# Kernel tuning notes

Measured on AMD Instinct MI355X. Metric: run time of the kernel, lower is better.

## Reference

```python
import jax, jax.numpy as jnp
import numpy as np

TEMP = 0.07
BASE_TEMP = 0.07


def setup_inputs() -> dict:
    key = jax.random.key(0)
    k1, k2 = jax.random.split(key)
    B, L, D = 512, 20, 128  # batch, num_classes, feat_size
    features = jax.random.normal(k1, (B, L, D), dtype=jnp.float32)
    # contrastive features are typically L2-normalized projections
    features = features / jnp.linalg.norm(features, axis=-1, keepdims=True)
    labels = jax.random.randint(k2, (B, L), 0, 2).astype(jnp.int32)  # multi-hot
    return {"features": features, "labels": labels}


def reference(features, labels):
    # features: [B, L, D], labels: [B, L] multi-hot
    B, L, D = features.shape
    dt = features.dtype
    lab = labels.astype(dt).T                      # [L, B]
    feat = jnp.transpose(features, (1, 0, 2))      # [L, B, D]

    logits_mask = 1.0 - jnp.eye(B, dtype=dt)       # [B, B], zero diagonal
    # mask[c, i, j] = labels[i, c] * labels[j, c] * (i != j)
    mask = (lab[:, :, None] * lab[:, None, :]) * logits_mask  # [L, B, B]

    # anchor_dot_contrast[c, l, i, j] = f[l,i] . f[c,j] / T  -> exp, masked on (i,j)
    # Compute via one big N x N gram, N = L*B (same math, single GEMM).
    F = feat.reshape(L * B, D)
    E = jnp.exp((F @ F.T) / jnp.asarray(TEMP, dt)).reshape(L, B, L, B)  # E[l,i,c,j]
    tot = E.sum(axis=(0, 3))                       # [B(i), L(c)] : sum over l, all j
    diag = jnp.diagonal(E, axis1=1, axis2=3)       # [L(l), L(c), B(i)] : j == i terms
    # sum_exp_logits[c, i] = sum_{l, j != i} exp(f[l,i].f[c,j]/T)
    S = tot.T - diag.sum(axis=0)                   # [L(c), B(i)]

    # numerator[c, i, j] = f[c,i] . f[c,j] / T
    numerator = jnp.einsum('cid,cjd->cij', feat, feat) / jnp.asarray(TEMP, dt)  # [L,B,B]
    log_prob = numerator - jnp.log(S)[:, :, None]  # [L, B, B]

    mean_log_prob_pos = (mask * log_prob).sum(axis=(0, 2))  # [B]
    average = mask.sum(axis=(0, 2))                          # [B]
    average = jnp.where(average == 0, jnp.asarray(1.0, dt), average)
    mean_log_prob_pos = mean_log_prob_pos / average

    loss = -(TEMP / BASE_TEMP) * jnp.mean(mean_log_prob_pos)
    return loss
```

## Files before the change

kernel.cpp:

```cpp
#include <hip/hip_runtime.h>
#include <hip/hip_fp8.h>


#define NB 512
#define NL 20
#define NROW (NB * NL)
#define F8BYTES (NROW * 128)
#define SCALE 4.5398160f
#define TEMP_INV 14.285714285714286f

typedef float f32x4 __attribute__((ext_vector_type(4)));

static __device__ __forceinline__ unsigned char f2fp8(float x) {
  __hip_fp8_e4m3 q(x);
  return (unsigned char)q.__x;
}

static __device__ __forceinline__ float fexp2(float x) {
#if __has_builtin(__builtin_amdgcn_exp2f)
  return __builtin_amdgcn_exp2f(x);
#else
  return exp2f(x);
#endif
}

__global__ __launch_bounds__(256) void k_prep(const float* __restrict__ feat,
                                              const int* __restrict__ labels,
                                              unsigned char* __restrict__ f8,
                                              float* __restrict__ gp) {
  const int b = blockIdx.x;
  if (b < 640) {
    int t = b * 256 + threadIdx.x;
    int q = t & 15;
    int a = t >> 4;
    int l = a >> 9;
    int i = a & 511;
    const float* src = feat + (size_t)i * (NL * 128) + l * 128 + q * 8;
    float4 v0 = *(const float4*)src;
    float4 v1 = *(const float4*)(src + 4);
    unsigned long long u = 0;
    u |= (unsigned long long)f2fp8(v0.x * SCALE);
    u |= (unsigned long long)f2fp8(v0.y * SCALE) << 8;
    u |= (unsigned long long)f2fp8(v0.z * SCALE) << 16;
    u |= (unsigned long long)f2fp8(v0.w * SCALE) << 24;
    u |= (unsigned long long)f2fp8(v1.x * SCALE) << 32;
    u |= (unsigned long long)f2fp8(v1.y * SCALE) << 40;
    u |= (unsigned long long)f2fp8(v1.z * SCALE) << 48;
    u |= (unsigned long long)f2fp8(v1.w * SCALE) << 56;
    *(unsigned long long*)(f8 + (size_t)a * 128 + ((q ^ (a & 7)) << 3)) = u;
  } else {
    __shared__ float part[2][128];
    const int idx = b - 640;
    const int c = idx >> 4, grp = idx & 15;
    const int d = threadIdx.x & 127, half = threadIdx.x >> 7;
    const int i0 = grp * 32 + half * 16;
    float s = 0.f;
#pragma unroll
    for (int k = 0; k < 16; ++k) {
      int i = i0 + k;
      s += (float)labels[i * NL + c] * feat[(size_t)i * (NL * 128) + c * 128 + d];
    }
    part[half][d] = s;
    __syncthreads();
    if (half == 0) gp[(c * 16 + grp) * 128 + d] = part[0][d] + part[1][d];
  }
}

__global__ __launch_bounds__(64) void k_gram(const unsigned char* __restrict__ f8,
                                             float* __restrict__ Pr) {
  __shared__ unsigned char lds[4096];
  const int x = blockIdx.x;
  const int h = x & 1, sr = x >> 1;
  const int c = blockIdx.y;
  const int lane = threadIdx.x;
  const int fr = lane & 15, kg = lane >> 4;
  const int x8 = (fr & 7) << 3;

  long af[4][4];
#pragma unroll
  for (int kk = 0; kk < 4; ++kk)
#pragma unroll
    for (int m = 0; m < 4; ++m)
      af[kk][m] = *(const long*)(f8 + (size_t)(sr * 64 + m * 16 + fr) * 128 +
                                 ((kk * 32 + kg * 8) ^ x8));

  const unsigned char* gB = f8 + ((size_t)c * 512 + h * 256) * 128 + lane * 16;
  auto stage = [&](int buf, int t) {
    const unsigned char* g = gB + t * 2048;
    unsigned char* lb = lds + buf * 2048 + lane * 16;
    __builtin_amdgcn_global_load_lds(
        (const __attribute__((address_space(1))) unsigned int*)g,
        (__attribute__((address_space(3))) unsigned int*)lb, 16, 0, 0);
    __builtin_amdgcn_global_load_lds(
        (const __attribute__((address_space(1))) unsigned int*)(g + 1024),
        (__attribute__((address_space(3))) unsigned int*)(lb + 1024), 16, 0, 0);
  };

  stage(0, 0);
  float esum[4][4] = {};

  const int d8 = sr & 7;
  const bool diagh = ((d8 >> 2) == h);
  const int td0 = (d8 & 3) * 4;

  for (int t = 0; t < 16; ++t) {
    asm volatile("" ::: "memory");
    if (t < 15) {
      stage((t + 1) & 1, t + 1);
      asm volatile("s_waitcnt vmcnt(2)" ::: "memory");
    } else {
      asm volatile("s_waitcnt vmcnt(0)" ::: "memory");
    }

    const unsigned char* lb = lds + (t & 1) * 2048;
    f32x4 acc[4] = {};
#pragma unroll
    for (int kk = 0; kk < 4; ++kk) {
      long bf = *(const long*)(lb + fr * 128 + ((kk * 32 + kg * 8) ^ x8));
#pragma unroll
      for (int m = 0; m < 4; ++m)
        acc[m] = __builtin_amdgcn_mfma_f32_16x16x32_fp8_fp8(af[kk][m], bf, acc[m], 0, 0, 0);
    }

    if (diagh && t >= td0 && t < td0 + 4) {
      const int mt = t - td0;
#pragma unroll
      for (int m = 0; m < 4; ++m)
#pragma unroll
        for (int reg = 0; reg < 4; ++reg) {
          float ex = fexp2(acc[m][reg]);
          if (m == mt && (kg * 4 + reg) == fr) ex = 0.f;
          esum[m][reg] += ex;
        }
    } else {
#pragma unroll
      for (int m = 0; m < 4; ++m)
#pragma unroll
        for (int reg = 0; reg < 4; ++reg)
          esum[m][reg] += fexp2(acc[m][reg]);
    }
  }

#pragma unroll
  for (int m = 0; m < 4; ++m)
#pragma unroll
    for (int reg = 0; reg < 4; ++reg) {
      float e = esum[m][reg];
      e += __shfl_xor(e, 1, 64); e += __shfl_xor(e, 2, 64);
      e += __shfl_xor(e, 4, 64); e += __shfl_xor(e, 8, 64);
      if (fr == 0)
        Pr[(((size_t)c * 2 + h) * 160 + sr) * 64 + m * 16 + kg * 4 + reg] = e;
    }
}

__global__ __launch_bounds__(256) void k_ws(const float* __restrict__ Pr,
                                            const float* __restrict__ feat,
                                            const float* __restrict__ gp,
                                            float* __restrict__ Slog,
                                            float* __restrict__ wnum) {
  const int b = blockIdx.x;
  if (b < 2560) {
    __shared__ float part[2][128];
    __shared__ float gsh[128];
    const int tid = threadIdx.x;
    const int c = (b * 4) >> 9;
    const int d = tid & 127, qh = tid >> 7;
    float s = 0.f;
#pragma unroll
    for (int q = 0; q < 8; ++q)
      s += gp[(c * 16 + qh * 8 + q) * 128 + d];
    part[qh][d] = s;
    __syncthreads();
    if (tid < 128) gsh[tid] = part[0][tid] + part[1][tid];
    __syncthreads();

    const int lane = tid & 63;
    const int p = b * 4 + (tid >> 6);
    const int i = p & 511;
    float2 f = *(const float2*)(feat + (size_t)i * (NL * 128) + c * 128 + lane * 2);
    float2 gv = *(const float2*)(gsh + lane * 2);
    float v = f.x * gv.x + f.y * gv.y;
#pragma unroll
    for (int sh = 1; sh < 64; sh <<= 1) v += __shfl_xor(v, sh, 64);
    if (lane == 0) wnum[p] = (v - 1.f) * TEMP_INV;
  } else {
    int idx = (b - 2560) * 256 + threadIdx.x;
    int c = idx >> 9, i = idx & 511;
    float s = 0.f;
#pragma unroll
    for (int l2 = 0; l2 < NL; ++l2) {
      const float* p2 = Pr + (((size_t)c * 2) * 160 + l2 * 8 + (i >> 6)) * 64 + (i & 63);
      s += p2[0] + p2[160 * 64];
    }
    Slog[idx] = logf(s);
  }
}

__global__ __launch_bounds__(512) void k_final(const float* __restrict__ Slog,
                                               const float* __restrict__ wnum,
                                               const int* __restrict__ labels,
                                               float* __restrict__ out) {
  __shared__ float cnt[NL];
  __shared__ float red[8];
  const int i = threadIdx.x;
  if (i < NL) cnt[i] = 0.f;
  __syncthreads();
  int lab[NL];
#pragma unroll
  for (int cI = 0; cI < NL; ++cI) lab[cI] = labels[i * NL + cI];
#pragma unroll
  for (int cI = 0; cI < NL; ++cI)
    if (lab[cI]) atomicAdd(&cnt[cI], 1.f);
  __syncthreads();
  float avg = 0.f, acc = 0.f;
#pragma unroll
  for (int cI = 0; cI < NL; ++cI) {
    if (lab[cI]) {
      float wgt = cnt[cI] - 1.f;
      avg += wgt;
      acc += wnum[cI * NB + i] - wgt * Slog[cI * NB + i];
    }
  }
  float v = acc / (avg == 0.f ? 1.f : avg);
#pragma unroll
  for (int s = 1; s < 64; s <<= 1) v += __shfl_xor(v, s, 64);
  if ((i & 63) == 0) red[i >> 6] = v;
  __syncthreads();
  if (i == 0) {
    float tot = 0.f;
#pragma unroll
    for (int k = 0; k < 8; ++k) tot += red[k];
    out[0] = -(tot / (float)NB);
  }
}

extern "C" void kernel_launch(void* const* d_in, const int* in_sizes, int n_in,
                              void* d_out, int out_size, void* d_ws, size_t ws_size,
                              hipStream_t stream) {
  const float* feat = (const float*)d_in[0];
  const int* labels = (const int*)d_in[1];
  float* out = (float*)d_out;
  unsigned char* ws = (unsigned char*)d_ws;
  unsigned char* f8 = ws;
  float* Pr = (float*)(ws + F8BYTES);
  float* gp = Pr + 20 * 2 * 160 * 64;
  float* Slog = gp + 320 * 128;
  float* wnum = Slog + NROW;

  k_prep<<<960, 256, 0, stream>>>(feat, labels, f8, gp);
  dim3 grid(320, 20);
  k_gram<<<grid, 64, 0, stream>>>(f8, Pr);
  k_ws<<<2600, 256, 0, stream>>>(Pr, feat, gp, Slog, wnum);
  k_final<<<1, 512, 0, stream>>>(Slog, wnum, labels, out);
}
```

Baseline: 50.16 us.

## Load gram B tiles directly into registers instead of staging through LDS

```diff
diff --git a/kernel.cpp b/kernel.cpp
--- a/kernel.cpp
+++ b/kernel.cpp
@@ -47,7 +47,7 @@
     u |= (unsigned long long)f2fp8(v1.y * SCALE) << 40;
     u |= (unsigned long long)f2fp8(v1.z * SCALE) << 48;
     u |= (unsigned long long)f2fp8(v1.w * SCALE) << 56;
-    *(unsigned long long*)(f8 + (size_t)a * 128 + ((q ^ (a & 7)) << 3)) = u;
+    *(unsigned long long*)(f8 + (size_t)a * 128 + q * 8) = u;
   } else {
     __shared__ float part[2][128];
     const int idx = b - 640;
@@ -68,13 +68,11 @@
 
 __global__ __launch_bounds__(64) void k_gram(const unsigned char* __restrict__ f8,
                                              float* __restrict__ Pr) {
-  __shared__ unsigned char lds[4096];
   const int x = blockIdx.x;
   const int h = x & 1, sr = x >> 1;
   const int c = blockIdx.y;
   const int lane = threadIdx.x;
   const int fr = lane & 15, kg = lane >> 4;
-  const int x8 = (fr & 7) << 3;
 
   long af[4][4];
 #pragma unroll
@@ -82,64 +80,55 @@
 #pragma unroll
     for (int m = 0; m < 4; ++m)
       af[kk][m] = *(const long*)(f8 + (size_t)(sr * 64 + m * 16 + fr) * 128 +
-                                 ((kk * 32 + kg * 8) ^ x8));
-
-  const unsigned char* gB = f8 + ((size_t)c * 512 + h * 256) * 128 + lane * 16;
-  auto stage = [&](int buf, int t) {
-    const unsigned char* g = gB + t * 2048;
-    unsigned char* lb = lds + buf * 2048 + lane * 16;
-    __builtin_amdgcn_global_load_lds(
-        (const __attribute__((address_space(1))) unsigned int*)g,
-        (__attribute__((address_space(3))) unsigned int*)lb, 16, 0, 0);
-    __builtin_amdgcn_global_load_lds(
-        (const __attribute__((address_space(1))) unsigned int*)(g + 1024),
-        (__attribute__((address_space(3))) unsigned int*)(lb + 1024), 16, 0, 0);
-  };
-
-  stage(0, 0);
+                                 kk * 32 + kg * 8);
+
+  const unsigned char* gL = f8 + ((size_t)(c * 512 + h * 256) + fr) * 128 + kg * 8;
+
+  long b0[4], b1[4];
+#define LOADB(DST, T)                                                        \
+  {                                                                          \
+    const unsigned char* g_ = gL + (size_t)(T) * 2048;                       \
+    _Pragma("unroll") for (int kk_ = 0; kk_ < 4; ++kk_)                      \
+        DST[kk_] = *(const long*)(g_ + kk_ * 32);                            \
+  }
+
   float esum[4][4] = {};
 
   const int d8 = sr & 7;
   const bool diagh = ((d8 >> 2) == h);
   const int td0 = (d8 & 3) * 4;
 
-  for (int t = 0; t < 16; ++t) {
-    asm volatile("" ::: "memory");
-    if (t < 15) {
-      stage((t + 1) & 1, t + 1);
-      asm volatile("s_waitcnt vmcnt(2)" ::: "memory");
-    } else {
-      asm volatile("s_waitcnt vmcnt(0)" ::: "memory");
-    }
-
-    const unsigned char* lb = lds + (t & 1) * 2048;
-    f32x4 acc[4] = {};
-#pragma unroll
-    for (int kk = 0; kk < 4; ++kk) {
-      long bf = *(const long*)(lb + fr * 128 + ((kk * 32 + kg * 8) ^ x8));
-#pragma unroll
-      for (int m = 0; m < 4; ++m)
-        acc[m] = __builtin_amdgcn_mfma_f32_16x16x32_fp8_fp8(af[kk][m], bf, acc[m], 0, 0, 0);
-    }
-
-    if (diagh && t >= td0 && t < td0 + 4) {
-      const int mt = t - td0;
-#pragma unroll
-      for (int m = 0; m < 4; ++m)
-#pragma unroll
-        for (int reg = 0; reg < 4; ++reg) {
-          float ex = fexp2(acc[m][reg]);
-          if (m == mt && (kg * 4 + reg) == fr) ex = 0.f;
-          esum[m][reg] += ex;
-        }
-    } else {
-#pragma unroll
-      for (int m = 0; m < 4; ++m)
-#pragma unroll
-        for (int reg = 0; reg < 4; ++reg)
-          esum[m][reg] += fexp2(acc[m][reg]);
-    }
-  }
+#define STEP(BU, BP, T)                                                      \
+  {                                                                          \
+    const int t_ = (T);                                                      \
+    if (t_ < 15) LOADB(BP, t_ + 1)                                           \
+    f32x4 acc[4] = {};                                                       \
+    _Pragma("unroll") for (int kk_ = 0; kk_ < 4; ++kk_)                      \
+    _Pragma("unroll") for (int m_ = 0; m_ < 4; ++m_)                         \
+        acc[m_] = __builtin_amdgcn_mfma_f32_16x16x32_fp8_fp8(af[kk_][m_],    \
+                      BU[kk_], acc[m_], 0, 0, 0);                            \
+    if (diagh && t_ >= td0 && t_ < td0 + 4) {                                \
+      const int mt_ = t_ - td0;                                              \
+      _Pragma("unroll") for (int m_ = 0; m_ < 4; ++m_)                       \
+      _Pragma("unroll") for (int r_ = 0; r_ < 4; ++r_) {                     \
+        float ex = fexp2(acc[m_][r_]);                                       \
+        if (m_ == mt_ && (kg * 4 + r_) == fr) ex = 0.f;                      \
+        esum[m_][r_] += ex;                                                  \
+      }                                                                      \
+    } else {                                                                 \
+      _Pragma("unroll") for (int m_ = 0; m_ < 4; ++m_)                       \
+      _Pragma("unroll") for (int r_ = 0; r_ < 4; ++r_)                       \
+          esum[m_][r_] += fexp2(acc[m_][r_]);                                \
+    }                                                                        \
+  }
+
+  LOADB(b0, 0)
+  for (int tt = 0; tt < 8; ++tt) {
+    STEP(b0, b1, 2 * tt)
+    STEP(b1, b0, 2 * tt + 1)
+  }
+#undef STEP
+#undef LOADB
 
 #pragma unroll
   for (int m = 0; m < 4; ++m)
```

After: 86.29 us. 1.72x slower.
